# Kernel tuning notes

Hardware: AMD Instinct MI355X
Metric: run time of the kernel (lower is better)

## Reference

```python
import jax, jax.numpy as jnp
import numpy as np

DIM = 1024
NH = 16
HD = DIM // NH  # 64
NT = max(1, int(NH * 0.25))  # 4 time heads
NS = NH - NT                 # 12 space heads
SCALE = HD ** (-0.5)


def setup_inputs() -> dict:
    key = jax.random.key(0)
    ks = jax.random.split(key, 8)
    B, T = 2, 2048
    init = 0.02
    return {
        "x": jax.random.normal(ks[0], (B, T, DIM), dtype=jnp.float32),
        # weights stored as (in, out); torch Linear y = x @ W.T is equivalent
        "Wqt": jax.random.normal(ks[1], (DIM, NT * HD), dtype=jnp.float32) * init,
        "Wkt": jax.random.normal(ks[2], (DIM, NT * HD), dtype=jnp.float32) * init,
        "Wqs": jax.random.normal(ks[3], (DIM, NS * HD), dtype=jnp.float32) * init,
        "Wks": jax.random.normal(ks[4], (DIM, NS * HD), dtype=jnp.float32) * init,
        "Wv": jax.random.normal(ks[5], (DIM, DIM), dtype=jnp.float32) * init,
        "Wout": jax.random.normal(ks[6], (DIM, DIM), dtype=jnp.float32) * init,
        "bout": jnp.zeros((DIM,), dtype=jnp.float32),
        "w_sigma": jnp.zeros((1,), dtype=jnp.float32),
    }


def reference(x, Wqt, Wkt, Wqs, Wks, Wv, Wout, bout, w_sigma):
    B, T, D = x.shape
    Qt = (x @ Wqt).reshape(B, T, NT, HD)
    Kt = (x @ Wkt).reshape(B, T, NT, HD)
    Qs = (x @ Wqs).reshape(B, T, NS, HD)
    Ks = (x @ Wks).reshape(B, T, NS, HD)
    st = jnp.einsum('bthd,bshd->bths', Qt, Kt)  # [B,T,NT,T]
    ss = jnp.einsum('bthd,bshd->bths', Qs, Ks)  # [B,T,NS,T]
    sig = jax.nn.sigmoid(w_sigma)  # shape (1,), broadcasts
    score = jnp.concatenate([-sig * st, ss], axis=2) * SCALE  # [B,T,NH,T]
    attn = jax.nn.softmax(score, axis=-1)
    V = (x @ Wv).reshape(B, T, NH, HD)
    ctx = jnp.einsum('bths,bshd->bthd', attn, V).reshape(B, T, D)
    return ctx @ Wout + bout
```

## Files before the change

### kernel.cpp

```cpp
#include <hip/hip_runtime.h>
#include <hip/hip_bf16.h>

typedef __bf16 bf16_t;
typedef __bf16 bf16x4 __attribute__((ext_vector_type(4)));
typedef __bf16 bf16x8 __attribute__((ext_vector_type(8)));
typedef float  f32x4  __attribute__((ext_vector_type(4)));

#define DIM     1024
#define NHEAD   16
#define HDIM    64
#define NTIME   4
#define TSEQ    2048
#define NBATCH  2
#define SCALE_F 0.125f
#define LOG2E   1.4426950408889634f

#define GLL(gp, lp) __builtin_amdgcn_global_load_lds( \
    (const __attribute__((address_space(1))) unsigned int*)(const void*)(gp), \
    (__attribute__((address_space(3))) unsigned int*)(void*)(lp), 16, 0, 0)

#define OFF_WQKVT 0UL
#define OFF_WOUTT (OFF_WQKVT + 3072UL*1024UL*2UL)
#define OFF_Q     (OFF_WOUTT + 1024UL*1024UL*2UL)
#define OFF_K     (OFF_Q  + 2UL*16UL*2048UL*64UL*2UL)
#define OFF_VT    (OFF_K  + 2UL*16UL*2048UL*64UL*2UL)
#define OFF_CTX   (OFF_VT + 2UL*16UL*2048UL*64UL*2UL)

__global__ void prep_wqkv_t(const float* __restrict__ Wqt, const float* __restrict__ Wkt,
                            const float* __restrict__ Wqs, const float* __restrict__ Wks,
                            const float* __restrict__ Wv,  bf16_t* __restrict__ WqkvT) {
    __shared__ float T[64][65];
    const int n0 = blockIdx.x * 64;
    const int k0 = blockIdx.y * 64;
    const int region = n0 >> 10;
    const int cc = n0 & 1023;
    const int h = cc >> 6;
    const float* src; int ncols, col0;
    if (region == 2) { src = Wv; ncols = 1024; col0 = cc; }
    else if (h < NTIME) { src = (region == 0) ? Wqt : Wkt; ncols = NTIME * HDIM; col0 = h * HDIM; }
    else                { src = (region == 0) ? Wqs : Wks; ncols = (NHEAD - NTIME) * HDIM; col0 = (h - NTIME) * HDIM; }

    const int tc = threadIdx.x & 63, tr = threadIdx.x >> 6;
#pragma unroll
    for (int i = 0; i < 16; ++i) {
        int kl = tr * 16 + i;
        T[kl][tc] = src[(size_t)(k0 + kl) * ncols + col0 + tc];
    }
    __syncthreads();
#pragma unroll
    for (int i = 0; i < 16; ++i) {
        int nl = tr * 16 + i;
        WqkvT[(size_t)(n0 + nl) * 1024 + k0 + tc] = (bf16_t)T[tc][nl];
    }
}

__global__ void prep_wout_t(const float* __restrict__ Wout, bf16_t* __restrict__ WoutT) {
    __shared__ float T[64][65];
    const int n0 = blockIdx.x * 64;
    const int k0 = blockIdx.y * 64;
    const int tc = threadIdx.x & 63, tr = threadIdx.x >> 6;
#pragma unroll
    for (int i = 0; i < 16; ++i) {
        int kl = tr * 16 + i;
        T[kl][tc] = Wout[(size_t)(k0 + kl) * 1024 + n0 + tc];
    }
    __syncthreads();
#pragma unroll
    for (int i = 0; i < 16; ++i) {
        int nl = tr * 16 + i;
        WoutT[(size_t)(n0 + nl) * 1024 + k0 + tc] = (bf16_t)T[tc][nl];
    }
}

__global__ void prep_x(const float* __restrict__ x, bf16_t* __restrict__ Xb) {
    int i = blockIdx.x * 256 + threadIdx.x;
    const float4* s = (const float4*)(x + (size_t)i * 8);
    float4 a = s[0], b = s[1];
    bf16x8 v;
    v[0] = (bf16_t)a.x; v[1] = (bf16_t)a.y; v[2] = (bf16_t)a.z; v[3] = (bf16_t)a.w;
    v[4] = (bf16_t)b.x; v[5] = (bf16_t)b.y; v[6] = (bf16_t)b.z; v[7] = (bf16_t)b.w;
    *(bf16x8*)(Xb + (size_t)i * 8) = v;
}

template<int MODE, int NB>
__global__ __launch_bounds__(256)
void gemm_bf16(const bf16_t* __restrict__ Ab, const bf16_t* __restrict__ Bt,
               bf16_t* __restrict__ Qb, bf16_t* __restrict__ Kb, bf16_t* __restrict__ Vt,
               float* __restrict__ Cout, const float* __restrict__ bias)
{
    __shared__ __align__(16) bf16_t As[128][64];
    __shared__ __align__(16) bf16_t Bs[128][64];

    const int cpx = gridDim.x >> 3;
    const int l = (blockIdx.x & 7) * cpx + (blockIdx.x >> 3);
    const int m0 = (l / NB) * 128, n0 = (l % NB) * 128;

    const int tid  = threadIdx.x;
    const int lane = tid & 63;
    const int wave = tid >> 6;
    const int wm = (wave >> 1) * 64, wn = (wave & 1) * 64;
    const int g = lane >> 4, lr = lane & 15;

    f32x4 acc[4][4];
#pragma unroll
    for (int i = 0; i < 4; ++i)
#pragma unroll
        for (int j = 0; j < 4; ++j) acc[i][j] = f32x4{0.f, 0.f, 0.f, 0.f};

    for (int k0 = 0; k0 < 1024; k0 += 64) {
        __syncthreads();
#pragma unroll
        for (int c = 0; c < 4; ++c) {
            int idx  = tid + c * 256;
            int row  = idx >> 3;
            int csrc = (idx & 7) ^ (row & 7);
            GLL(Ab + (size_t)(m0 + row) * 1024 + k0 + csrc * 8,
                (char*)&As[0][0] + (c * 256 + wave * 64) * 16);
            GLL(Bt + (size_t)(n0 + row) * 1024 + k0 + csrc * 8,
                (char*)&Bs[0][0] + (c * 256 + wave * 64) * 16);
        }
        __syncthreads();

#pragma unroll
        for (int kk = 0; kk < 2; ++kk) {
            bf16x8 afr[4], bfr[4];
#pragma unroll
            for (int f = 0; f < 4; ++f) {
                int ra = wm + f * 16 + lr;
                afr[f] = *(const bf16x8*)((const char*)&As[0][0] + ra * 128 + (((kk * 4 + g) ^ (ra & 7)) << 4));
                int rb = wn + f * 16 + lr;
                bfr[f] = *(const bf16x8*)((const char*)&Bs[0][0] + rb * 128 + (((kk * 4 + g) ^ (rb & 7)) << 4));
            }
#pragma unroll
            for (int fm = 0; fm < 4; ++fm)
#pragma unroll
                for (int fn = 0; fn < 4; ++fn)
                    acc[fm][fn] = __builtin_amdgcn_mfma_f32_16x16x32_bf16(bfr[fn], afr[fm], acc[fm][fn], 0, 0, 0);
        }
    }

    const int region = n0 >> 10;
#pragma unroll
    for (int fm = 0; fm < 4; ++fm) {
        const int m = m0 + wm + fm * 16 + lr;
        const int b = m >> 11, t = m & 2047;
#pragma unroll
        for (int fn = 0; fn < 4; ++fn) {
            const int nb = n0 + wn + fn * 16 + g * 4;
            if constexpr (MODE == 1) {
                float4 bb = *(const float4*)(bias + nb);
                float4 v;
                v.x = acc[fm][fn][0] + bb.x;
                v.y = acc[fm][fn][1] + bb.y;
                v.z = acc[fm][fn][2] + bb.z;
                v.w = acc[fm][fn][3] + bb.w;
                *(float4*)(Cout + (size_t)m * DIM + nb) = v;
            } else {
                const int cc = nb & 1023;
                const int h = cc >> 6, d0 = cc & 63;
                const size_t bh = (size_t)(b * NHEAD + h);
                if (region == 2) {
#pragma unroll
                    for (int r = 0; r < 4; ++r)
                        Vt[(bh * HDIM + d0 + r) * TSEQ + t] = (bf16_t)acc[fm][fn][r];
                } else {
                    bf16x4 w;
#pragma unroll
                    for (int r = 0; r < 4; ++r) w[r] = (bf16_t)acc[fm][fn][r];
                    bf16_t* dst = (region == 0) ? Qb : Kb;
                    *(bf16x4*)(dst + (bh * TSEQ + t) * HDIM + d0) = w;
                }
            }
        }
    }
}

__global__ __launch_bounds__(512, 4)
void attn_kernel(const bf16_t* __restrict__ Qb, const bf16_t* __restrict__ Kb,
                 const bf16_t* __restrict__ Vt, bf16_t* __restrict__ ctx,
                 const float* __restrict__ w_sigma)
{
    __shared__ __align__(16) bf16_t Ktile[2][128][64];
    __shared__ __align__(16) bf16_t Vtile[2][64][128];
    __shared__ __align__(16) char   P2[8][2048];

    const int l    = ((blockIdx.x & 7) << 6) + (blockIdx.x >> 3);
    const int qc   = l & 15;
    const int bh   = l >> 4;
    const int h    = bh & 15;
    const int b    = bh >> 4;
    const int tid  = threadIdx.x;
    const int lane = tid & 63;
    const int wave = tid >> 6;
    const int g = lane >> 4, lr = lane & 15;
    const int q0 = qc * 128 + wave * 16;

    const float sig = 1.f / (1.f + __expf(-w_sigma[0]));
    const float fl2 = ((h < NTIME) ? (-sig * SCALE_F) : SCALE_F) * LOG2E;

    const bf16_t* Qp = Qb + (size_t)bh * TSEQ * HDIM;
    const bf16_t* Kp = Kb + (size_t)bh * TSEQ * HDIM;
    const bf16_t* Vp = Vt + (size_t)bh * HDIM * TSEQ;

    bf16x8 qa0 = *(const bf16x8*)(Qp + (size_t)(q0 + lr) * HDIM + g * 8);
    bf16x8 qa1 = *(const bf16x8*)(Qp + (size_t)(q0 + lr) * HDIM + 32 + g * 8);
#pragma unroll
    for (int e = 0; e < 8; ++e) {
        qa0[e] = (bf16_t)((float)qa0[e] * fl2);
        qa1[e] = (bf16_t)((float)qa1[e] * fl2);
    }

    f32x4 o[4];
#pragma unroll
    for (int n = 0; n < 4; ++n) o[n] = f32x4{0.f, 0.f, 0.f, 0.f};
    float l_part = 0.f;

    char* const P2w = &P2[wave][0];
    const int qsw = (lr & 7) << 4;

    const int krow = (tid >> 3);
    const int kcg  = tid & 7;
    const int vrow = (tid >> 4);
    const int vcg  = tid & 15;

    auto stage = [&](int s0, int buf) {
#pragma unroll
        for (int j = 0; j < 2; ++j) {
            int kr = j * 64 + krow;
            GLL(Kp + (size_t)(s0 + kr) * HDIM + ((kcg ^ (kr & 7)) << 3),
                (char*)&Ktile[buf][0][0] + (j * 512 + wave * 64) * 16);
            int vr = j * 32 + vrow;
            GLL(Vp + (size_t)vr * TSEQ + s0 + ((vcg ^ (vr & 15)) << 3),
                (char*)&Vtile[buf][0][0] + (j * 512 + wave * 64) * 16);
        }
    };

    auto half_compute = [&](const char* Kt, const char* Vc, int hf) {
        __builtin_amdgcn_s_setprio(1);
#pragma unroll
        for (int st = 0; st < 4; ++st) {
            const int srow = hf * 64 + st * 16 + lr;
            const int rs7 = lr & 7;
            bf16x8 kb0 = *(const bf16x8*)(Kt + srow * 128 + ((g ^ rs7) << 4));
            bf16x8 kb1 = *(const bf16x8*)(Kt + srow * 128 + (((4 + g) ^ rs7) << 4));
            f32x4 z = f32x4{0.f, 0.f, 0.f, 0.f};
            z = __builtin_amdgcn_mfma_f32_16x16x32_bf16(kb0, qa0, z, 0, 0, 0);
            z = __builtin_amdgcn_mfma_f32_16x16x32_bf16(kb1, qa1, z, 0, 0, 0);
            float p0 = __builtin_amdgcn_exp2f(z[0]);
            float p1 = __builtin_amdgcn_exp2f(z[1]);
            float p2 = __builtin_amdgcn_exp2f(z[2]);
            float p3 = __builtin_amdgcn_exp2f(z[3]);
            bf16x4 w;
            w[0] = (bf16_t)p0; w[1] = (bf16_t)p1; w[2] = (bf16_t)p2; w[3] = (bf16_t)p3;
            *(bf16x4*)(P2w + lr * 128 + ((st * 32 + g * 8) ^ qsw)) = w;
            l_part += (p0 + p1) + (p2 + p3);
        }
        __builtin_amdgcn_s_setprio(0);

        asm volatile("s_waitcnt lgkmcnt(0)" ::: "memory");
        __builtin_amdgcn_sched_barrier(0);

        __builtin_amdgcn_s_setprio(1);
#pragma unroll
        for (int kc = 0; kc < 2; ++kc) {
            bf16x8 pa = *(const bf16x8*)(P2w + lr * 128 + ((kc * 64 + g * 16) ^ qsw));
#pragma unroll
            for (int n = 0; n < 4; ++n) {
                const int row = n * 16 + lr;
                bf16x8 vb = *(const bf16x8*)(Vc + row * 256 + (((hf * 8 + kc * 4 + g) ^ (row & 15)) << 4));
                o[n] = __builtin_amdgcn_mfma_f32_16x16x32_bf16(vb, pa, o[n], 0, 0, 0);
            }
        }
        __builtin_amdgcn_s_setprio(0);
    };

    const char* const K0 = (const char*)&Ktile[0][0][0];
    const char* const K1 = (const char*)&Ktile[1][0][0];
    const char* const V0 = (const char*)&Vtile[0][0][0];
    const char* const V1 = (const char*)&Vtile[1][0][0];

    stage(0, 0);
    __syncthreads();

    for (int it = 0; it < 8; ++it) {
        const int s0 = it * 256;
        stage(s0 + 128, 1);
        half_compute(K0, V0, 0);
        half_compute(K0, V0, 1);
        __syncthreads();
        if (s0 + 256 < TSEQ) stage(s0 + 256, 0);
        half_compute(K1, V1, 0);
        half_compute(K1, V1, 1);
        __syncthreads();
    }

    float lf = l_part;
    lf += __shfl_xor(lf, 16, 64);
    lf += __shfl_xor(lf, 32, 64);
    float linv = 1.f / lf;

    const int t = q0 + lr;
#pragma unroll
    for (int n = 0; n < 4; ++n) {
        bf16x4 w;
#pragma unroll
        for (int r = 0; r < 4; ++r) w[r] = (bf16_t)(o[n][r] * linv);
        *(bf16x4*)(ctx + ((size_t)(b * TSEQ + t)) * DIM + h * HDIM + n * 16 + g * 4) = w;
    }
}

extern "C" void kernel_launch(void* const* d_in, const int* in_sizes, int n_in,
                              void* d_out, int out_size, void* d_ws, size_t ws_size,
                              hipStream_t stream) {
    const float* x    = (const float*)d_in[0];
    const float* Wqt  = (const float*)d_in[1];
    const float* Wkt  = (const float*)d_in[2];
    const float* Wqs  = (const float*)d_in[3];
    const float* Wks  = (const float*)d_in[4];
    const float* Wv   = (const float*)d_in[5];
    const float* Wout = (const float*)d_in[6];
    const float* bout = (const float*)d_in[7];
    const float* wsig = (const float*)d_in[8];
    (void)in_sizes; (void)n_in; (void)out_size; (void)ws_size;

    char* ws = (char*)d_ws;
    bf16_t* WqkvT = (bf16_t*)(ws + OFF_WQKVT);
    bf16_t* WoutT = (bf16_t*)(ws + OFF_WOUTT);
    bf16_t* Qb    = (bf16_t*)(ws + OFF_Q);
    bf16_t* Kb    = (bf16_t*)(ws + OFF_K);
    bf16_t* Vt    = (bf16_t*)(ws + OFF_VT);
    bf16_t* ctx   = (bf16_t*)(ws + OFF_CTX);
    bf16_t* Xb    = ctx;
    float*  out   = (float*)d_out;

    prep_wqkv_t<<<dim3(48, 16), 256, 0, stream>>>(Wqt, Wkt, Wqs, Wks, Wv, WqkvT);
    prep_wout_t<<<dim3(16, 16), 256, 0, stream>>>(Wout, WoutT);
    prep_x<<<2048, 256, 0, stream>>>(x, Xb);

    gemm_bf16<0, 24><<<768, 256, 0, stream>>>(Xb, WqkvT, Qb, Kb, Vt, nullptr, nullptr);

    attn_kernel<<<512, 512, 0, stream>>>(Qb, Kb, Vt, ctx, wsig);

    gemm_bf16<1, 8><<<256, 256, 0, stream>>>(ctx, WoutT, nullptr, nullptr, nullptr, out, bout);
}
```

Measured before the change: 124.7 us.

## Fuse prep kernels and give each attention wave two query tiles

The three preprocessing kernels (x cast, QKV weight transpose, Wout transpose) become one launch that picks its job from the block index, removing two launch overheads. The attention kernel drops from 8 to 4 waves per block, and each wave now handles 32 query rows (two 16-row tiles), so every K and V fragment read from LDS feeds twice as many MFMAs. The cost is more accumulator and Q registers per wave and fewer waves per block to hide latency. Staging loops are adjusted so 256 threads still fill the K/V tiles.

```diff
diff --git a/kernel.cpp b/kernel.cpp
--- a/kernel.cpp
+++ b/kernel.cpp
@@ -26,60 +26,63 @@
 #define OFF_VT    (OFF_K  + 2UL*16UL*2048UL*64UL*2UL)
 #define OFF_CTX   (OFF_VT + 2UL*16UL*2048UL*64UL*2UL)
 
-__global__ void prep_wqkv_t(const float* __restrict__ Wqt, const float* __restrict__ Wkt,
-                            const float* __restrict__ Wqs, const float* __restrict__ Wks,
-                            const float* __restrict__ Wv,  bf16_t* __restrict__ WqkvT) {
+__global__ void prep_all(const float* __restrict__ x,
+                         const float* __restrict__ Wqt, const float* __restrict__ Wkt,
+                         const float* __restrict__ Wqs, const float* __restrict__ Wks,
+                         const float* __restrict__ Wv,  const float* __restrict__ Wout,
+                         bf16_t* __restrict__ Xb, bf16_t* __restrict__ WqkvT,
+                         bf16_t* __restrict__ WoutT) {
     __shared__ float T[64][65];
-    const int n0 = blockIdx.x * 64;
-    const int k0 = blockIdx.y * 64;
-    const int region = n0 >> 10;
-    const int cc = n0 & 1023;
-    const int h = cc >> 6;
-    const float* src; int ncols, col0;
-    if (region == 2) { src = Wv; ncols = 1024; col0 = cc; }
-    else if (h < NTIME) { src = (region == 0) ? Wqt : Wkt; ncols = NTIME * HDIM; col0 = h * HDIM; }
-    else                { src = (region == 0) ? Wqs : Wks; ncols = (NHEAD - NTIME) * HDIM; col0 = (h - NTIME) * HDIM; }
-
+    const int bid = blockIdx.x;
+    if (bid < 2048) {
+        int i = bid * 256 + threadIdx.x;
+        const float4* s = (const float4*)(x + (size_t)i * 8);
+        float4 a = s[0], b2 = s[1];
+        bf16x8 v;
+        v[0] = (bf16_t)a.x;  v[1] = (bf16_t)a.y;  v[2] = (bf16_t)a.z;  v[3] = (bf16_t)a.w;
+        v[4] = (bf16_t)b2.x; v[5] = (bf16_t)b2.y; v[6] = (bf16_t)b2.z; v[7] = (bf16_t)b2.w;
+        *(bf16x8*)(Xb + (size_t)i * 8) = v;
+        return;
+    }
     const int tc = threadIdx.x & 63, tr = threadIdx.x >> 6;
-#pragma unroll
-    for (int i = 0; i < 16; ++i) {
-        int kl = tr * 16 + i;
-        T[kl][tc] = src[(size_t)(k0 + kl) * ncols + col0 + tc];
-    }
-    __syncthreads();
-#pragma unroll
-    for (int i = 0; i < 16; ++i) {
-        int nl = tr * 16 + i;
-        WqkvT[(size_t)(n0 + nl) * 1024 + k0 + tc] = (bf16_t)T[tc][nl];
-    }
-}
-
-__global__ void prep_wout_t(const float* __restrict__ Wout, bf16_t* __restrict__ WoutT) {
-    __shared__ float T[64][65];
-    const int n0 = blockIdx.x * 64;
-    const int k0 = blockIdx.y * 64;
-    const int tc = threadIdx.x & 63, tr = threadIdx.x >> 6;
-#pragma unroll
-    for (int i = 0; i < 16; ++i) {
-        int kl = tr * 16 + i;
-        T[kl][tc] = Wout[(size_t)(k0 + kl) * 1024 + n0 + tc];
-    }
-    __syncthreads();
-#pragma unroll
-    for (int i = 0; i < 16; ++i) {
-        int nl = tr * 16 + i;
-        WoutT[(size_t)(n0 + nl) * 1024 + k0 + tc] = (bf16_t)T[tc][nl];
-    }
-}
-
-__global__ void prep_x(const float* __restrict__ x, bf16_t* __restrict__ Xb) {
-    int i = blockIdx.x * 256 + threadIdx.x;
-    const float4* s = (const float4*)(x + (size_t)i * 8);
-    float4 a = s[0], b = s[1];
-    bf16x8 v;
-    v[0] = (bf16_t)a.x; v[1] = (bf16_t)a.y; v[2] = (bf16_t)a.z; v[3] = (bf16_t)a.w;
-    v[4] = (bf16_t)b.x; v[5] = (bf16_t)b.y; v[6] = (bf16_t)b.z; v[7] = (bf16_t)b.w;
-    *(bf16x8*)(Xb + (size_t)i * 8) = v;
+    if (bid < 2816) {
+        const int l = bid - 2048;
+        const int n0 = (l % 48) * 64;
+        const int k0 = (l / 48) * 64;
+        const int region = n0 >> 10;
+        const int cc = n0 & 1023;
+        const int h = cc >> 6;
+        const float* src; int ncols, col0;
+        if (region == 2) { src = Wv; ncols = 1024; col0 = cc; }
+        else if (h < NTIME) { src = (region == 0) ? Wqt : Wkt; ncols = NTIME * HDIM; col0 = h * HDIM; }
+        else                { src = (region == 0) ? Wqs : Wks; ncols = (NHEAD - NTIME) * HDIM; col0 = (h - NTIME) * HDIM; }
+#pragma unroll
+        for (int i = 0; i < 16; ++i) {
+            int kl = tr * 16 + i;
+            T[kl][tc] = src[(size_t)(k0 + kl) * ncols + col0 + tc];
+        }
+        __syncthreads();
+#pragma unroll
+        for (int i = 0; i < 16; ++i) {
+            int nl = tr * 16 + i;
+            WqkvT[(size_t)(n0 + nl) * 1024 + k0 + tc] = (bf16_t)T[tc][nl];
+        }
+    } else {
+        const int l = bid - 2816;
+        const int n0 = (l % 16) * 64;
+        const int k0 = (l / 16) * 64;
+#pragma unroll
+        for (int i = 0; i < 16; ++i) {
+            int kl = tr * 16 + i;
+            T[kl][tc] = Wout[(size_t)(k0 + kl) * 1024 + n0 + tc];
+        }
+        __syncthreads();
+#pragma unroll
+        for (int i = 0; i < 16; ++i) {
+            int nl = tr * 16 + i;
+            WoutT[(size_t)(n0 + nl) * 1024 + k0 + tc] = (bf16_t)T[tc][nl];
+        }
+    }
 }
 
 template<int MODE, int NB>
@@ -175,14 +178,14 @@
     }
 }
 
-__global__ __launch_bounds__(512, 4)
+__global__ __launch_bounds__(256, 2)
 void attn_kernel(const bf16_t* __restrict__ Qb, const bf16_t* __restrict__ Kb,
                  const bf16_t* __restrict__ Vt, bf16_t* __restrict__ ctx,
                  const float* __restrict__ w_sigma)
 {
     __shared__ __align__(16) bf16_t Ktile[2][128][64];
     __shared__ __align__(16) bf16_t Vtile[2][64][128];
-    __shared__ __align__(16) char   P2[8][2048];
+    __shared__ __align__(16) char   P2[4][4096];
 
     const int l    = ((blockIdx.x & 7) << 6) + (blockIdx.x >> 3);
     const int qc   = l & 15;
@@ -193,7 +196,7 @@
     const int lane = tid & 63;
     const int wave = tid >> 6;
     const int g = lane >> 4, lr = lane & 15;
-    const int q0 = qc * 128 + wave * 16;
+    const int q0 = qc * 128 + wave * 32;
 
     const float sig = 1.f / (1.f + __expf(-w_sigma[0]));
     const float fl2 = ((h < NTIME) ? (-sig * SCALE_F) : SCALE_F) * LOG2E;
@@ -204,34 +207,38 @@
 
     bf16x8 qa0 = *(const bf16x8*)(Qp + (size_t)(q0 + lr) * HDIM + g * 8);
     bf16x8 qa1 = *(const bf16x8*)(Qp + (size_t)(q0 + lr) * HDIM + 32 + g * 8);
+    bf16x8 qb0 = *(const bf16x8*)(Qp + (size_t)(q0 + 16 + lr) * HDIM + g * 8);
+    bf16x8 qb1 = *(const bf16x8*)(Qp + (size_t)(q0 + 16 + lr) * HDIM + 32 + g * 8);
 #pragma unroll
     for (int e = 0; e < 8; ++e) {
         qa0[e] = (bf16_t)((float)qa0[e] * fl2);
         qa1[e] = (bf16_t)((float)qa1[e] * fl2);
-    }
-
-    f32x4 o[4];
-#pragma unroll
-    for (int n = 0; n < 4; ++n) o[n] = f32x4{0.f, 0.f, 0.f, 0.f};
-    float l_part = 0.f;
+        qb0[e] = (bf16_t)((float)qb0[e] * fl2);
+        qb1[e] = (bf16_t)((float)qb1[e] * fl2);
+    }
+
+    f32x4 oA[4], oB[4];
+#pragma unroll
+    for (int n = 0; n < 4; ++n) { oA[n] = f32x4{0.f,0.f,0.f,0.f}; oB[n] = f32x4{0.f,0.f,0.f,0.f}; }
+    float lpA = 0.f, lpB = 0.f;
 
     char* const P2w = &P2[wave][0];
     const int qsw = (lr & 7) << 4;
 
-    const int krow = (tid >> 3);
+    const int krow = tid >> 3;
     const int kcg  = tid & 7;
-    const int vrow = (tid >> 4);
+    const int vrow = tid >> 4;
     const int vcg  = tid & 15;
 
     auto stage = [&](int s0, int buf) {
 #pragma unroll
-        for (int j = 0; j < 2; ++j) {
-            int kr = j * 64 + krow;
+        for (int j = 0; j < 4; ++j) {
+            int kr = j * 32 + krow;
             GLL(Kp + (size_t)(s0 + kr) * HDIM + ((kcg ^ (kr & 7)) << 3),
-                (char*)&Ktile[buf][0][0] + (j * 512 + wave * 64) * 16);
-            int vr = j * 32 + vrow;
+                (char*)&Ktile[buf][0][0] + (j * 256 + wave * 64) * 16);
+            int vr = j * 16 + vrow;
             GLL(Vp + (size_t)vr * TSEQ + s0 + ((vcg ^ (vr & 15)) << 3),
-                (char*)&Vtile[buf][0][0] + (j * 512 + wave * 64) * 16);
+                (char*)&Vtile[buf][0][0] + (j * 256 + wave * 64) * 16);
         }
     };
 
@@ -243,17 +250,26 @@
             const int rs7 = lr & 7;
             bf16x8 kb0 = *(const bf16x8*)(Kt + srow * 128 + ((g ^ rs7) << 4));
             bf16x8 kb1 = *(const bf16x8*)(Kt + srow * 128 + (((4 + g) ^ rs7) << 4));
-            f32x4 z = f32x4{0.f, 0.f, 0.f, 0.f};
-            z = __builtin_amdgcn_mfma_f32_16x16x32_bf16(kb0, qa0, z, 0, 0, 0);
-            z = __builtin_amdgcn_mfma_f32_16x16x32_bf16(kb1, qa1, z, 0, 0, 0);
-            float p0 = __builtin_amdgcn_exp2f(z[0]);
-            float p1 = __builtin_amdgcn_exp2f(z[1]);
-            float p2 = __builtin_amdgcn_exp2f(z[2]);
-            float p3 = __builtin_amdgcn_exp2f(z[3]);
-            bf16x4 w;
-            w[0] = (bf16_t)p0; w[1] = (bf16_t)p1; w[2] = (bf16_t)p2; w[3] = (bf16_t)p3;
-            *(bf16x4*)(P2w + lr * 128 + ((st * 32 + g * 8) ^ qsw)) = w;
-            l_part += (p0 + p1) + (p2 + p3);
+            f32x4 zA = f32x4{0.f,0.f,0.f,0.f}, zB = f32x4{0.f,0.f,0.f,0.f};
+            zA = __builtin_amdgcn_mfma_f32_16x16x32_bf16(kb0, qa0, zA, 0, 0, 0);
+            zA = __builtin_amdgcn_mfma_f32_16x16x32_bf16(kb1, qa1, zA, 0, 0, 0);
+            zB = __builtin_amdgcn_mfma_f32_16x16x32_bf16(kb0, qb0, zB, 0, 0, 0);
+            zB = __builtin_amdgcn_mfma_f32_16x16x32_bf16(kb1, qb1, zB, 0, 0, 0);
+            float a0 = __builtin_amdgcn_exp2f(zA[0]);
+            float a1 = __builtin_amdgcn_exp2f(zA[1]);
+            float a2 = __builtin_amdgcn_exp2f(zA[2]);
+            float a3 = __builtin_amdgcn_exp2f(zA[3]);
+            float b0 = __builtin_amdgcn_exp2f(zB[0]);
+            float b1 = __builtin_amdgcn_exp2f(zB[1]);
+            float b2 = __builtin_amdgcn_exp2f(zB[2]);
+            float b3 = __builtin_amdgcn_exp2f(zB[3]);
+            bf16x4 wA, wB;
+            wA[0] = (bf16_t)a0; wA[1] = (bf16_t)a1; wA[2] = (bf16_t)a2; wA[3] = (bf16_t)a3;
+            wB[0] = (bf16_t)b0; wB[1] = (bf16_t)b1; wB[2] = (bf16_t)b2; wB[3] = (bf16_t)b3;
+            *(bf16x4*)(P2w +        lr * 128 + ((st * 32 + g * 8) ^ qsw)) = wA;
+            *(bf16x4*)(P2w + 2048 + lr * 128 + ((st * 32 + g * 8) ^ qsw)) = wB;
+            lpA += (a0 + a1) + (a2 + a3);
+            lpB += (b0 + b1) + (b2 + b3);
         }
         __builtin_amdgcn_s_setprio(0);
 
@@ -263,12 +279,14 @@
         __builtin_amdgcn_s_setprio(1);
 #pragma unroll
         for (int kc = 0; kc < 2; ++kc) {
-            bf16x8 pa = *(const bf16x8*)(P2w + lr * 128 + ((kc * 64 + g * 16) ^ qsw));
+            bf16x8 paA = *(const bf16x8*)(P2w +        lr * 128 + ((kc * 64 + g * 16) ^ qsw));
+            bf16x8 paB = *(const bf16x8*)(P2w + 2048 + lr * 128 + ((kc * 64 + g * 16) ^ qsw));
 #pragma unroll
             for (int n = 0; n < 4; ++n) {
                 const int row = n * 16 + lr;
                 bf16x8 vb = *(const bf16x8*)(Vc + row * 256 + (((hf * 8 + kc * 4 + g) ^ (row & 15)) << 4));
-                o[n] = __builtin_amdgcn_mfma_f32_16x16x32_bf16(vb, pa, o[n], 0, 0, 0);
+                oA[n] = __builtin_amdgcn_mfma_f32_16x16x32_bf16(vb, paA, oA[n], 0, 0, 0);
+                oB[n] = __builtin_amdgcn_mfma_f32_16x16x32_bf16(vb, paB, oB[n], 0, 0, 0);
             }
         }
         __builtin_amdgcn_s_setprio(0);
@@ -294,18 +312,24 @@
         __syncthreads();
     }
 
-    float lf = l_part;
-    lf += __shfl_xor(lf, 16, 64);
-    lf += __shfl_xor(lf, 32, 64);
-    float linv = 1.f / lf;
-
-    const int t = q0 + lr;
+    float lfA = lpA, lfB = lpB;
+    lfA += __shfl_xor(lfA, 16, 64);
+    lfA += __shfl_xor(lfA, 32, 64);
+    lfB += __shfl_xor(lfB, 16, 64);
+    lfB += __shfl_xor(lfB, 32, 64);
+    float liA = 1.f / lfA, liB = 1.f / lfB;
+
+    const int tA = q0 + lr, tB = q0 + 16 + lr;
 #pragma unroll
     for (int n = 0; n < 4; ++n) {
-        bf16x4 w;
-#pragma unroll
-        for (int r = 0; r < 4; ++r) w[r] = (bf16_t)(o[n][r] * linv);
-        *(bf16x4*)(ctx + ((size_t)(b * TSEQ + t)) * DIM + h * HDIM + n * 16 + g * 4) = w;
+        bf16x4 wA, wB;
+#pragma unroll
+        for (int r = 0; r < 4; ++r) {
+            wA[r] = (bf16_t)(oA[n][r] * liA);
+            wB[r] = (bf16_t)(oB[n][r] * liB);
+        }
+        *(bf16x4*)(ctx + ((size_t)(b * TSEQ + tA)) * DIM + h * HDIM + n * 16 + g * 4) = wA;
+        *(bf16x4*)(ctx + ((size_t)(b * TSEQ + tB)) * DIM + h * HDIM + n * 16 + g * 4) = wB;
     }
 }
 
@@ -333,13 +357,11 @@
     bf16_t* Xb    = ctx;
     float*  out   = (float*)d_out;
 
-    prep_wqkv_t<<<dim3(48, 16), 256, 0, stream>>>(Wqt, Wkt, Wqs, Wks, Wv, WqkvT);
-    prep_wout_t<<<dim3(16, 16), 256, 0, stream>>>(Wout, WoutT);
-    prep_x<<<2048, 256, 0, stream>>>(x, Xb);
+    prep_all<<<3072, 256, 0, stream>>>(x, Wqt, Wkt, Wqs, Wks, Wv, Wout, Xb, WqkvT, WoutT);
 
     gemm_bf16<0, 24><<<768, 256, 0, stream>>>(Xb, WqkvT, Qb, Kb, Vt, nullptr, nullptr);
 
-    attn_kernel<<<512, 512, 0, stream>>>(Qb, Kb, Vt, ctx, wsig);
+    attn_kernel<<<512, 256, 0, stream>>>(Qb, Kb, Vt, ctx, wsig);
 
     gemm_bf16<1, 8><<<256, 256, 0, stream>>>(ctx, WoutT, nullptr, nullptr, nullptr, out, bout);
 }
```

Result: faster. 119.5 us (-4.2%).
